# Performance work log

Hardware: AMD Instinct MI355X
Metric: run time of the kernel (lower is better)

Reference implementation:

```python
import jax, jax.numpy as jnp
import numpy as np

LEN = 4          # self.lenth: 4x4 window grid -> max seq len 16
HEADS = 16
SHIFT = LEN // 2 # cyclic shift of lenth//2 in generate_mask


def _build_mask(n):
    # generate_mask(h=heads//2, w=2, p=LEN, shift=SHIFT), type != 'W'
    h, w, p = HEADS // 2, 2, LEN
    s = p - SHIFT
    m = np.zeros((h, w, p, p, p, p), dtype=bool)
    m[-1, :, :s, :, s:, :] = True
    m[-1, :, s:, :, :s, :] = True
    m[:, -1, :, :s, :, s:] = True
    m[:, -1, :, s:, :, :s] = True
    # 'w1 w2 p1 p2 p3 p4 -> 1 (w1 w2) (p1 p2) (p3 p4)' (contiguous merge)
    m = m.reshape(1, h * w, p * p, p * p)
    return jnp.asarray(m[:, :, :n, :n])


def _rel_indices(n):
    cord = np.array([[i, j] for i in range(LEN) for j in range(LEN)])  # (16,2)
    rel = cord[:n, None, :] - cord[None, :n, :] + LEN - 1              # (n,n,2)
    return rel[..., 0], rel[..., 1]


def setup_inputs() -> dict:
    key = jax.random.key(0)
    ks = jax.random.split(key, 6)
    b, n, dim = 4096, 16, 512
    inner = HEADS * 64  # heads * dim_head = 1024
    return {
        "x": jax.random.normal(ks[0], (b, n, dim), dtype=jnp.float32),
        "w_qkv": jax.random.normal(ks[1], (3 * inner, dim), dtype=jnp.float32) * 0.02,
        "b_qkv": jax.random.normal(ks[2], (3 * inner,), dtype=jnp.float32) * 0.02,
        "w_proj": jax.random.normal(ks[3], (dim, inner), dtype=jnp.float32) * 0.02,
        "b_proj": jax.random.normal(ks[4], (dim,), dtype=jnp.float32) * 0.02,
        "rel_pos": jax.random.normal(ks[5], (HEADS, 2 * LEN - 1, 2 * LEN - 1), dtype=jnp.float32) * 0.02,
    }


def reference(x, w_qkv, b_qkv, w_proj, b_proj, rel_pos):
    b, n, _ = x.shape
    h = HEADS
    # type != 'W' -> cyclic shift along tokens
    x = jnp.roll(x, -(n // 2), axis=1)
    qkv = x @ w_qkv.T + b_qkv                       # (b, n, 3*inner)
    q, k, v = jnp.split(qkv, 3, axis=-1)
    split = lambda t: t.reshape(b, n, h, -1).transpose(0, 2, 1, 3)  # b h n d
    q, k, v = split(q), split(k), split(v)
    scale = q.shape[-1] ** -0.5
    dots = jnp.einsum('bhid,bhjd->bhij', q, k) * scale
    r0, r1 = _rel_indices(n)
    dots = dots + rel_pos[:, r0, r1][None]          # (1, h, n, n) rel-pos bias
    mask = _build_mask(n)                           # (1, h, n, n) bool
    dots = jnp.where(mask, -jnp.inf, dots)
    attn = jax.nn.softmax(dots, axis=-1)
    out = jnp.einsum('bhij,bhjd->bhid', attn, v)
    out = out.transpose(0, 2, 1, 3).reshape(b, n, -1)  # (b, n, inner)
    return out @ w_proj.T + b_proj
```

## Files before the change

### kernel.cpp

```cpp
#include <hip/hip_runtime.h>
#include <stdint.h>


typedef __attribute__((ext_vector_type(8))) short frag8;
typedef __attribute__((ext_vector_type(4))) float frag4f;

__device__ __forceinline__ uint16_t f2bf(float f) {
  union { float f; uint32_t i; } x; x.f = f;
  uint32_t r = x.i + 0x7fffu + ((x.i >> 16) & 1u);
  return (uint16_t)(r >> 16);
}


__global__ __launch_bounds__(256)
void k_cvt(const float* __restrict__ src, uint16_t* __restrict__ dst, int n4, int ok)
{
  if (!ok) return;
  int i = blockIdx.x * 256 + threadIdx.x;
  const int stride = gridDim.x * 256;
  for (; i < n4; i += stride) {
    float4 v = ((const float4*)src)[i];
    ushort4 o;
    o.x = f2bf(v.x); o.y = f2bf(v.y); o.z = f2bf(v.z); o.w = f2bf(v.w);
    ((ushort4*)dst)[i] = o;
  }
}


struct SmemEpi  { uint16_t q[128][72]; uint16_t k[128][72];
                  uint16_t vT[64][136]; uint16_t p[8][16][24]; };
union Smem1 { uint8_t g[2][20480]; SmemEpi e; };

__global__ __launch_bounds__(256, 2)
void k_qkv_attn(const uint16_t* __restrict__ xb, const uint16_t* __restrict__ wqkvb,
                const float* __restrict__ b_qkv, const float* __restrict__ rel_pos,
                uint16_t* __restrict__ attn16, int ws_ok)
{
  __shared__ Smem1 sm;
  const int bid  = blockIdx.x;
  const int h    = bid & 15;
  const int mt   = bid >> 4;
  const int t    = threadIdx.x;
  const int lane = t & 63;
  const int wv   = t >> 6;
  const int l15  = lane & 15;
  const int quad = lane >> 4;
  const int wr   = wv & 1;
  const int wc   = wv >> 1;

  if (!ws_ok) {
    #pragma unroll
    for (int i = 0; i < 32; ++i) {
      const int local = t + 256 * i;
      const int row = local >> 6, col = local & 63;
      attn16[(mt * 128 + row) * 1024 + h * 64 + col] = 0;
    }
    return;
  }

  const int slot_g = (lane & 3) ^ ((lane >> 3) & 3);
  const uint16_t* sp[5];
  int ldsoff[5];
  #pragma unroll
  for (int o = 0; o < 5; ++o) {
    const int c = wv * 5 + o;
    const int rloc = c * 16 + (lane >> 2);
    if (c < 8) {
      const int g = mt * 128 + rloc;
      const int srow = (g & ~15) | ((g + 8) & 15);
      sp[o] = xb + srow * 512 + slot_g * 8;
    } else {
      const int cb = rloc - 128;
      const int gc = (cb < 64) ? (h * 64 + cb)
                   : (cb < 128) ? (1024 + h * 64 + (cb - 64))
                                : (2048 + h * 64 + (cb - 128));
      sp[o] = wqkvb + gc * 512 + slot_g * 8;
    }
    ldsoff[o] = c * 1024;
  }

  frag4f acc[4][6];
  #pragma unroll
  for (int a = 0; a < 4; ++a)
    #pragma unroll
    for (int b = 0; b < 6; ++b) acc[a][b] = (frag4f)0.0f;

  auto STAGE = [&](int buf, int kk) {
    #pragma unroll
    for (int o = 0; o < 5; ++o)
      __builtin_amdgcn_global_load_lds(
          (const __attribute__((address_space(1))) void*)(sp[o] + kk * 32),
          (__attribute__((address_space(3))) void*)(sm.g[buf] + ldsoff[o]),
          16, 0, 0);
  };

  STAGE(0, 0);
  __syncthreads();

  const int xq = quad ^ ((l15 >> 1) & 3);
  for (int kk = 0; kk < 16; ++kk) {
    const int cur = kk & 1;
    if (kk < 15) STAGE(cur ^ 1, kk + 1);

    const uint8_t* base = sm.g[cur];
    frag8 af[4], bf[6];
    #pragma unroll
    for (int rt = 0; rt < 4; ++rt)
      af[rt] = *(const frag8*)(base + (wr * 64 + rt * 16 + l15) * 64 + xq * 16);
    #pragma unroll
    for (int ct = 0; ct < 6; ++ct)
      bf[ct] = *(const frag8*)(base + 8192 + ((wc * 6 + ct) * 16 + l15) * 64 + xq * 16);
    #pragma unroll
    for (int rt = 0; rt < 4; ++rt)
      #pragma unroll
      for (int ct = 0; ct < 6; ++ct)
        acc[rt][ct] = __builtin_amdgcn_mfma_f32_16x16x32_bf16(af[rt], bf[ct], acc[rt][ct], 0, 0, 0);
    __syncthreads();
  }

  #pragma unroll
  for (int ct = 0; ct < 6; ++ct) {
    const int C = (wc * 6 + ct) * 16 + l15;
    const int gc = (C < 64) ? (h * 64 + C)
                 : (C < 128) ? (1024 + h * 64 + (C - 64))
                             : (2048 + h * 64 + (C - 128));
    const float bias = b_qkv[gc];
    #pragma unroll
    for (int rt = 0; rt < 4; ++rt) {
      #pragma unroll
      for (int r = 0; r < 4; ++r) {
        const int row = wr * 64 + rt * 16 + quad * 4 + r;
        const uint16_t val = f2bf(acc[rt][ct][r] + bias);
        if (C < 64)       sm.e.q[row][C] = val;
        else if (C < 128) sm.e.k[row][C - 64] = val;
        else              sm.e.vT[C - 128][row] = val;
      }
    }
  }
  __syncthreads();

  const float scl = 0.125f;
  #pragma unroll
  for (int bbi = 0; bbi < 2; ++bbi) {
    const int bb = wv * 2 + bbi;
    frag8 a0 = *(const frag8*)&sm.e.q[bb * 16 + l15][quad * 8];
    frag8 a1 = *(const frag8*)&sm.e.q[bb * 16 + l15][32 + quad * 8];
    frag8 b0 = *(const frag8*)&sm.e.k[bb * 16 + l15][quad * 8];
    frag8 b1 = *(const frag8*)&sm.e.k[bb * 16 + l15][32 + quad * 8];
    frag4f s = (frag4f)0.0f;
    s = __builtin_amdgcn_mfma_f32_16x16x32_bf16(a0, b0, s, 0, 0, 0);
    s = __builtin_amdgcn_mfma_f32_16x16x32_bf16(a1, b1, s, 0, 0, 0);
    const int j = l15;
    #pragma unroll
    for (int r = 0; r < 4; ++r) {
      const int i = quad * 4 + r;
      const int r0 = (i >> 2) - (j >> 2) + 3;
      const int r1 = (i & 3) - (j & 3) + 3;
      const float bias = rel_pos[h * 49 + r0 * 7 + r1];
      const bool msk = ((h >= 14) && (((i >> 2) < 2) != ((j >> 2) < 2))) ||
                       ((h & 1)  && (((i & 3) < 2) != ((j & 3) < 2)));
      float v = msk ? -1e30f : (s[r] * scl + bias);
      float m = v;
      m = fmaxf(m, __shfl_xor(m, 1));
      m = fmaxf(m, __shfl_xor(m, 2));
      m = fmaxf(m, __shfl_xor(m, 4));
      m = fmaxf(m, __shfl_xor(m, 8));
      float e = __expf(v - m);
      float su = e;
      su += __shfl_xor(su, 1);
      su += __shfl_xor(su, 2);
      su += __shfl_xor(su, 4);
      su += __shfl_xor(su, 8);
      sm.e.p[bb][i][j] = f2bf(e / su);
    }
  }
  __syncthreads();

  #pragma unroll
  for (int bbi = 0; bbi < 2; ++bbi) {
    const int bb = wv * 2 + bbi;
    frag8 ap;
    if (quad < 2) ap = *(const frag8*)&sm.e.p[bb][l15][quad * 8];
    else          ap = (frag8)0;
    #pragma unroll
    for (int dt = 0; dt < 4; ++dt) {
      frag8 bv = *(const frag8*)&sm.e.vT[dt * 16 + l15][bb * 16 + (quad & 1) * 8];
      frag4f o = (frag4f)0.0f;
      o = __builtin_amdgcn_mfma_f32_16x16x32_bf16(ap, bv, o, 0, 0, 0);
      #pragma unroll
      for (int r = 0; r < 4; ++r) {
        const int grow = mt * 128 + bb * 16 + quad * 4 + r;
        attn16[grow * 1024 + h * 64 + dt * 16 + l15] = f2bf(o[r]);
      }
    }
  }
}


__global__ __launch_bounds__(512, 4)
void k_proj(const uint16_t* __restrict__ attn16, const uint16_t* __restrict__ wprojb,
            const float* __restrict__ b_proj, float* __restrict__ out, int ws_ok)
{
  __shared__ uint8_t smraw[2 * 36864];
  const int mt   = blockIdx.x;
  const int t    = threadIdx.x;
  const int lane = t & 63;
  const int wv   = t >> 6;
  const int l15  = lane & 15;
  const int quad = lane >> 4;

  if (!ws_ok) {
    for (int i = t; i < 64 * 512; i += 512) {
      const int row = i >> 9, col = i & 511;
      out[(mt * 64 + row) * 512 + col] = b_proj[col];
    }
    return;
  }

  const int cnt = (wv < 4) ? 5 : 4;
  const int c0  = (wv < 4) ? wv * 5 : 20 + (wv - 4) * 4;
  const int slot_g = (lane & 3) ^ ((lane >> 3) & 3);

  const uint16_t* gp[5];
  int lds_off[5];
  #pragma unroll
  for (int o = 0; o < 5; ++o) {
    int c = c0 + o;
    if (c > 35) c = 35;
    const int rloc = c * 16 + (lane >> 2);
    if (c < 4) {
      gp[o] = attn16 + (size_t)(mt * 64 + rloc) * 1024 + slot_g * 8;
    } else {
      gp[o] = wprojb + (size_t)(rloc - 64) * 1024 + slot_g * 8;
    }
    lds_off[o] = (c0 + o) * 1024;
  }

  frag4f acc[4][4];
  #pragma unroll
  for (int a = 0; a < 4; ++a)
    #pragma unroll
    for (int b = 0; b < 4; ++b) acc[a][b] = (frag4f)0.0f;

  auto STAGE = [&](int buf, int kk) {
    #pragma unroll
    for (int o = 0; o < 5; ++o)
      if (o < cnt)
        __builtin_amdgcn_global_load_lds(
            (const __attribute__((address_space(1))) void*)(gp[o] + kk * 32),
            (__attribute__((address_space(3))) void*)(smraw + buf * 36864 + lds_off[o]),
            16, 0, 0);
  };

  STAGE(0, 0);
  __syncthreads();

  const int xq = quad ^ ((l15 >> 1) & 3);
  for (int kk = 0; kk < 32; ++kk) {
    const int cur = kk & 1;
    if (kk < 31) STAGE(cur ^ 1, kk + 1);

    const uint16_t* As = (const uint16_t*)(smraw + cur * 36864);
    const uint16_t* Bs = (const uint16_t*)(smraw + cur * 36864 + 4096);
    frag8 af[4];
    #pragma unroll
    for (int rt = 0; rt < 4; ++rt)
      af[rt] = *(const frag8*)(As + (rt * 16 + l15) * 32 + xq * 8);
    #pragma unroll
    for (int ct = 0; ct < 4; ++ct) {
      frag8 bfr = *(const frag8*)(Bs + (wv * 64 + ct * 16 + l15) * 32 + xq * 8);
      #pragma unroll
      for (int rt = 0; rt < 4; ++rt)
        acc[rt][ct] = __builtin_amdgcn_mfma_f32_16x16x32_bf16(af[rt], bfr, acc[rt][ct], 0, 0, 0);
    }
    __syncthreads();
  }

  #pragma unroll
  for (int ct = 0; ct < 4; ++ct) {
    const int gcol = wv * 64 + ct * 16 + l15;
    const float bias = b_proj[gcol];
    #pragma unroll
    for (int rt = 0; rt < 4; ++rt) {
      #pragma unroll
      for (int r = 0; r < 4; ++r) {
        const int grow = mt * 64 + rt * 16 + quad * 4 + r;
        out[grow * 512 + gcol] = acc[rt][ct][r] + bias;
      }
    }
  }
}


extern "C" void kernel_launch(void* const* d_in, const int* in_sizes, int n_in,
                              void* d_out, int out_size, void* d_ws, size_t ws_size,
                              hipStream_t stream) {
  const float* x      = (const float*)d_in[0];
  const float* w_qkv  = (const float*)d_in[1];
  const float* b_qkv  = (const float*)d_in[2];
  const float* w_proj = (const float*)d_in[3];
  const float* b_proj = (const float*)d_in[4];
  const float* rel    = (const float*)d_in[5];

  uint16_t* xb     = (uint16_t*)d_ws;
  uint16_t* wqkvb  = xb + 33554432;
  uint16_t* wprojb = wqkvb + 1572864;
  const size_t ws_need = (size_t)(33554432 + 1572864 + 524288) * 2;
  const int ws_ok = (ws_size >= ws_need) ? 1 : 0;

  uint16_t* attn16 = (uint16_t*)d_out;
  float*    out    = (float*)d_out;

  k_cvt<<<dim3(4096), dim3(256), 0, stream>>>(x,      xb,     33554432 / 4, ws_ok);
  k_cvt<<<dim3(1536), dim3(256), 0, stream>>>(w_qkv,  wqkvb,  1572864 / 4,  ws_ok);
  k_cvt<<<dim3(512),  dim3(256), 0, stream>>>(w_proj, wprojb, 524288 / 4,   ws_ok);
  k_qkv_attn<<<dim3(512 * 16), dim3(256), 0, stream>>>(xb, wqkvb, b_qkv, rel, attn16, ws_ok);
  k_proj    <<<dim3(1024),     dim3(512), 0, stream>>>(attn16, wprojb, b_proj, out, ws_ok);
}
```

Baseline: 633.7 us.

## Use partial vmcnt waits in GEMM loops and shrink LDS for three blocks per CU

Replaces the full __syncthreads in both GEMM main loops with explicit s_waitcnt vmcnt(N) plus s_barrier, so the next stage's async global-to-LDS loads stay in flight while the current tile is consumed. It also shrinks LDS padding and reuses the q buffer for the softmax probabilities, which lets the launch bound ask for three blocks per CU in the QKV/attention kernel. The hand-tuned vmcnt counts rely on each wave's exact load count (per-wave differences in k_proj), and the tighter register budget from the higher occupancy target could cause spills.

```diff
diff --git a/kernel.cpp b/kernel.cpp
--- a/kernel.cpp
+++ b/kernel.cpp
@@ -10,6 +10,8 @@
   uint32_t r = x.i + 0x7fffu + ((x.i >> 16) & 1u);
   return (uint16_t)(r >> 16);
 }
+
+#define SCHED0() __builtin_amdgcn_sched_barrier(0)
 
 
 __global__ __launch_bounds__(256)
@@ -27,11 +29,11 @@
 }
 
 
-struct SmemEpi  { uint16_t q[128][72]; uint16_t k[128][72];
-                  uint16_t vT[64][136]; uint16_t p[8][16][24]; };
+struct SmemEpi  { uint16_t q[128][68]; uint16_t k[128][68];
+                  uint16_t vT[64][132]; };
 union Smem1 { uint8_t g[2][20480]; SmemEpi e; };
 
-__global__ __launch_bounds__(256, 2)
+__global__ __launch_bounds__(256, 3)
 void k_qkv_attn(const uint16_t* __restrict__ xb, const uint16_t* __restrict__ wqkvb,
                 const float* __restrict__ b_qkv, const float* __restrict__ rel_pos,
                 uint16_t* __restrict__ attn16, int ws_ok)
@@ -95,12 +97,21 @@
   };
 
   STAGE(0, 0);
-  __syncthreads();
 
   const int xq = quad ^ ((l15 >> 1) & 3);
   for (int kk = 0; kk < 16; ++kk) {
     const int cur = kk & 1;
-    if (kk < 15) STAGE(cur ^ 1, kk + 1);
+    if (kk < 15) {
+      STAGE(cur ^ 1, kk + 1);
+      SCHED0();
+      asm volatile("s_waitcnt vmcnt(5)" ::: "memory");
+    } else {
+      SCHED0();
+      asm volatile("s_waitcnt vmcnt(0)" ::: "memory");
+    }
+    SCHED0();
+    __builtin_amdgcn_s_barrier();
+    SCHED0();
 
     const uint8_t* base = sm.g[cur];
     frag8 af[4], bf[6];
@@ -115,7 +126,12 @@
       #pragma unroll
       for (int ct = 0; ct < 6; ++ct)
         acc[rt][ct] = __builtin_amdgcn_mfma_f32_16x16x32_bf16(af[rt], bf[ct], acc[rt][ct], 0, 0, 0);
-    __syncthreads();
+
+    SCHED0();
+    asm volatile("s_waitcnt lgkmcnt(0)" ::: "memory");
+    SCHED0();
+    __builtin_amdgcn_s_barrier();
+    SCHED0();
   }
 
   #pragma unroll
@@ -140,16 +156,29 @@
   __syncthreads();
 
   const float scl = 0.125f;
+  frag8 qa0[2], qa1[2], kb0[2], kb1[2];
+  frag4f s2[2];
   #pragma unroll
   for (int bbi = 0; bbi < 2; ++bbi) {
     const int bb = wv * 2 + bbi;
-    frag8 a0 = *(const frag8*)&sm.e.q[bb * 16 + l15][quad * 8];
-    frag8 a1 = *(const frag8*)&sm.e.q[bb * 16 + l15][32 + quad * 8];
-    frag8 b0 = *(const frag8*)&sm.e.k[bb * 16 + l15][quad * 8];
-    frag8 b1 = *(const frag8*)&sm.e.k[bb * 16 + l15][32 + quad * 8];
+    qa0[bbi] = *(const frag8*)&sm.e.q[bb * 16 + l15][quad * 8];
+    qa1[bbi] = *(const frag8*)&sm.e.q[bb * 16 + l15][32 + quad * 8];
+    kb0[bbi] = *(const frag8*)&sm.e.k[bb * 16 + l15][quad * 8];
+    kb1[bbi] = *(const frag8*)&sm.e.k[bb * 16 + l15][32 + quad * 8];
+  }
+  #pragma unroll
+  for (int bbi = 0; bbi < 2; ++bbi) {
     frag4f s = (frag4f)0.0f;
-    s = __builtin_amdgcn_mfma_f32_16x16x32_bf16(a0, b0, s, 0, 0, 0);
-    s = __builtin_amdgcn_mfma_f32_16x16x32_bf16(a1, b1, s, 0, 0, 0);
+    s = __builtin_amdgcn_mfma_f32_16x16x32_bf16(qa0[bbi], kb0[bbi], s, 0, 0, 0);
+    s = __builtin_amdgcn_mfma_f32_16x16x32_bf16(qa1[bbi], kb1[bbi], s, 0, 0, 0);
+    s2[bbi] = s;
+  }
+  __syncthreads();
+
+  uint16_t (*pp)[16][20] = (uint16_t (*)[16][20])sm.e.q;
+  #pragma unroll
+  for (int bbi = 0; bbi < 2; ++bbi) {
+    const int bb = wv * 2 + bbi;
     const int j = l15;
     #pragma unroll
     for (int r = 0; r < 4; ++r) {
@@ -159,7 +188,7 @@
       const float bias = rel_pos[h * 49 + r0 * 7 + r1];
       const bool msk = ((h >= 14) && (((i >> 2) < 2) != ((j >> 2) < 2))) ||
                        ((h & 1)  && (((i & 3) < 2) != ((j & 3) < 2)));
-      float v = msk ? -1e30f : (s[r] * scl + bias);
+      float v = msk ? -1e30f : (s2[bbi][r] * scl + bias);
       float m = v;
       m = fmaxf(m, __shfl_xor(m, 1));
       m = fmaxf(m, __shfl_xor(m, 2));
@@ -171,7 +200,7 @@
       su += __shfl_xor(su, 2);
       su += __shfl_xor(su, 4);
       su += __shfl_xor(su, 8);
-      sm.e.p[bb][i][j] = f2bf(e / su);
+      pp[bb][i][j] = f2bf(e / su);
     }
   }
   __syncthreads();
@@ -180,7 +209,7 @@
   for (int bbi = 0; bbi < 2; ++bbi) {
     const int bb = wv * 2 + bbi;
     frag8 ap;
-    if (quad < 2) ap = *(const frag8*)&sm.e.p[bb][l15][quad * 8];
+    if (quad < 2) ap = *(const frag8*)&pp[bb][l15][quad * 8];
     else          ap = (frag8)0;
     #pragma unroll
     for (int dt = 0; dt < 4; ++dt) {
@@ -253,12 +282,22 @@
   };
 
   STAGE(0, 0);
-  __syncthreads();
 
   const int xq = quad ^ ((l15 >> 1) & 3);
   for (int kk = 0; kk < 32; ++kk) {
     const int cur = kk & 1;
-    if (kk < 31) STAGE(cur ^ 1, kk + 1);
+    if (kk < 31) {
+      STAGE(cur ^ 1, kk + 1);
+      SCHED0();
+      if (wv < 4) asm volatile("s_waitcnt vmcnt(5)" ::: "memory");
+      else        asm volatile("s_waitcnt vmcnt(4)" ::: "memory");
+    } else {
+      SCHED0();
+      asm volatile("s_waitcnt vmcnt(0)" ::: "memory");
+    }
+    SCHED0();
+    __builtin_amdgcn_s_barrier();
+    SCHED0();
 
     const uint16_t* As = (const uint16_t*)(smraw + cur * 36864);
     const uint16_t* Bs = (const uint16_t*)(smraw + cur * 36864 + 4096);
@@ -273,7 +312,12 @@
       for (int rt = 0; rt < 4; ++rt)
         acc[rt][ct] = __builtin_amdgcn_mfma_f32_16x16x32_bf16(af[rt], bfr, acc[rt][ct], 0, 0, 0);
     }
-    __syncthreads();
+
+    SCHED0();
+    asm volatile("s_waitcnt lgkmcnt(0)" ::: "memory");
+    SCHED0();
+    __builtin_amdgcn_s_barrier();
+    SCHED0();
   }
 
   #pragma unroll
```

Result: faster. 606.0 us (-4.4%).
